# Kernel optimization log

Hardware: AMD Instinct MI355X
Metric: run time of the kernel (lower is better)

Reference implementation:

```python
import jax, jax.numpy as jnp
import numpy as np
import math

D_MODEL = 2048
NUM_HEADS = 32
NUM_KV_HEADS = 8
D_K = D_MODEL // NUM_HEADS  # 64
GROUPS = NUM_HEADS // NUM_KV_HEADS  # 4
WINDOW = 512
ROPE_BASE = 10000.0


def setup_inputs() -> dict:
    key = jax.random.key(0)
    ks = jax.random.split(key, 5)
    B, T = 2, 2048
    x = jax.random.normal(ks[0], (B, T, D_MODEL), dtype=jnp.float32)
    s = 0.02  # typical init scale to keep logits sane
    Wq = jax.random.normal(ks[1], (D_MODEL, D_MODEL), dtype=jnp.float32) * s
    Wk = jax.random.normal(ks[2], (NUM_KV_HEADS * D_K, D_MODEL), dtype=jnp.float32) * s
    Wv = jax.random.normal(ks[3], (NUM_KV_HEADS * D_K, D_MODEL), dtype=jnp.float32) * s
    Wo = jax.random.normal(ks[4], (D_MODEL, D_MODEL), dtype=jnp.float32) * s
    return {"x": x, "Wq": Wq, "Wk": Wk, "Wv": Wv, "Wo": Wo}


def _rotate_half(t):
    half = t.shape[-1] // 2
    return jnp.concatenate([-t[..., half:], t[..., :half]], axis=-1)


def _rope_cos_sin(T, dtype):
    inv_freq = 1.0 / (ROPE_BASE ** (jnp.arange(0, D_K, 2, dtype=jnp.float32) / D_K))
    pos = jnp.arange(T, dtype=jnp.float32)
    freqs = pos[:, None] * inv_freq[None, :]            # [T, D_K/2]
    emb = jnp.concatenate([freqs, freqs], axis=-1)       # [T, D_K]
    return jnp.cos(emb).astype(dtype)[None, None], jnp.sin(emb).astype(dtype)[None, None]


def reference(x, Wq, Wk, Wv, Wo):
    B, T, D = x.shape
    # Projections (nn.Linear: x @ W.T)
    Q = (x @ Wq.T).reshape(B, T, NUM_HEADS, D_K).transpose(0, 2, 1, 3)     # [B,H,T,dk]
    K = (x @ Wk.T).reshape(B, T, NUM_KV_HEADS, D_K).transpose(0, 2, 1, 3)  # [B,KV,T,dk]
    V = (x @ Wv.T).reshape(B, T, NUM_KV_HEADS, D_K).transpose(0, 2, 1, 3)
    # RoPE
    cos, sin = _rope_cos_sin(T, x.dtype)
    Q = Q * cos + _rotate_half(Q) * sin
    K = K * cos + _rotate_half(K) * sin
    # GQA: fold group dim into Q instead of repeat_interleave on K/V (same math)
    Qg = Q.reshape(B, NUM_KV_HEADS, GROUPS, T, D_K)
    scale = math.sqrt(D_K)
    scores = jnp.einsum('bhgqd,bhkd->bhgqk', Qg, K) / scale  # [B,KV,G,T,T]
    # sliding-window causal mask: valid iff 0 <= q_pos - k_pos < WINDOW
    pos = jnp.arange(T)
    dist = pos[:, None] - pos[None, :]
    win_mask = (dist < 0) | (dist >= WINDOW)
    scores = jnp.where(win_mask[None, None, None], -jnp.inf, scores)
    attn = jax.nn.softmax(scores, axis=-1)
    out = jnp.einsum('bhgqk,bhkd->bhgqd', attn, V)
    out = out.reshape(B, NUM_HEADS, T, D_K).transpose(0, 2, 1, 3).reshape(B, T, D)
    return out @ Wo.T
```

## Files before the change

kernel.cpp:

```cpp
#include <hip/hip_runtime.h>
#include <hip/hip_bf16.h>
#include <cstdint>
#include <cstddef>

typedef __attribute__((ext_vector_type(4))) float f32x4;
typedef __attribute__((ext_vector_type(8))) short bf16x8;
typedef __attribute__((ext_vector_type(4))) int i32x4;
typedef void __attribute__((address_space(1)))* as1_void_p;
typedef void __attribute__((address_space(3)))* as3_void_p;

#define T_SEQ 2048
#define D_MODEL 2048
#define NUM_HEADS 32
#define NUM_KV 8
#define GROUPS 4
#define DK 64
#define WINDOW 512
#define BATCH 2

#define NEG_BIG (-30000.0f)

__device__ __forceinline__ unsigned short f2b(float f) {
    unsigned int u = __builtin_bit_cast(unsigned int, f);
    u = (u + 0x7FFFu + ((u >> 16) & 1u)) >> 16;
    return (unsigned short)u;
}

__device__ __forceinline__ unsigned int cvtpk_bf16(float lo, float hi) {
    unsigned int r;
    asm("v_cvt_pk_bf16_f32 %0, %1, %2" : "=v"(r) : "v"(lo), "v"(hi));
    return r;
}

__device__ __forceinline__ void load_lds16(const void* g, void* l) {
    __builtin_amdgcn_global_load_lds((as1_void_p)(uintptr_t)g,
                                     (as3_void_p)(unsigned int)(uintptr_t)l,
                                     16, 0, 0);
}

#define CAST_N0 8388608
#define CAST_N1 12582912
#define CAST_N2 13631488
#define CAST_N3 14680064
#define CAST_N4 18874368
__global__ void cast_all_kernel(const float* __restrict__ x, const float* __restrict__ wq,
                                const float* __restrict__ wk, const float* __restrict__ wv,
                                const float* __restrict__ wo, unsigned short* __restrict__ dst) {
    int i = (blockIdx.x * blockDim.x + threadIdx.x) * 4;
    const int stride = gridDim.x * blockDim.x * 4;
    for (; i < CAST_N4; i += stride) {
        const float* src;
        int off;
        if (i < CAST_N0)      { src = x;  off = i; }
        else if (i < CAST_N1) { src = wq; off = i - CAST_N0; }
        else if (i < CAST_N2) { src = wk; off = i - CAST_N1; }
        else if (i < CAST_N3) { src = wv; off = i - CAST_N2; }
        else                  { src = wo; off = i - CAST_N3; }
        const float4 v = *(const float4*)(src + off);
        ushort4 o;
        o.x = f2b(v.x); o.y = f2b(v.y); o.z = f2b(v.z); o.w = f2b(v.w);
        *(ushort4*)(dst + i) = o;
    }
}

__global__ void rope_table_kernel(float* __restrict__ ct, float* __restrict__ st) {
    int i = blockIdx.x * blockDim.x + threadIdx.x;
    int t = i >> 5, j = i & 31;
    const float kln = 0.28782313662425556f;
    float inv = __expf(-(float)j * kln);
    if (j == 0) inv = 1.0f;
    float ang = (float)t * inv;
    float s, c;
    sincosf(ang, &s, &c);
    ct[i] = c; st[i] = s;
}

__global__ __launch_bounds__(512, 2) void gemm_qkv_rope(
    const unsigned short* __restrict__ A, const unsigned short* __restrict__ Bw,
    const float* __restrict__ ct, const float* __restrict__ st,
    unsigned short* __restrict__ Qb, unsigned short* __restrict__ Kb,
    unsigned short* __restrict__ Vt) {
    __shared__ __align__(16) unsigned short lds[65536];
    const int bid = blockIdx.x;
    const int xcd = bid & 7;
    const int l = bid >> 3;
    const int stl = l >> 2;
    const int w = l & 3;
    const int tile_m = xcd * 2 + (w >> 1);
    const int tile_n = stl * 2 + (w & 1);

    const int tid = threadIdx.x;
    const int lane = tid & 63;
    const int wid = tid >> 6;
    const int wr = wid >> 2, wc = wid & 3;
    const int lrow = lane & 15;
    const int g = lane >> 4;
    const int arow = tile_m * 256, brow = tile_n * 256;

    f32x4 acc[8][4] = {};

#define QSTAGE(SRC, ROWBASE, KCOL, USHOFF)                                     \
    { _Pragma("unroll") for (int u = 0; u < 2; ++u) {                          \
        const int gi = u * 512 + tid;                                          \
        const int row_ = gi >> 2, sl_ = gi & 3;                                \
        const int sc_ = (sl_ ^ ((row_ >> 1) & 3)) << 3;                        \
        load_lds16(SRC + (size_t)((ROWBASE) + row_) * 2048 + (KCOL) + sc_,     \
                   (char*)&lds[USHOFF] + gi * 16); } }

    QSTAGE(A, arow, 0,  0)     QSTAGE(Bw, brow, 0,  8192)
    QSTAGE(A, arow, 32, 16384) QSTAGE(Bw, brow, 32, 24576)
    QSTAGE(A, arow, 64, 32768) QSTAGE(Bw, brow, 64, 40960)
    asm volatile("s_waitcnt vmcnt(8)" ::: "memory");
    __builtin_amdgcn_sched_barrier(0);
    __builtin_amdgcn_s_barrier();

    for (int t = 0; t < 64; ++t) {
        const int cb = (t & 3) * 16384;
        const int sb = ((t + 3) & 3) * 16384;
        bf16x8 af[8], bfr[4];
#pragma unroll
        for (int m = 0; m < 8; ++m) {
            const int R = wr * 128 + m * 16 + lrow;
            af[m] = *(const bf16x8*)&lds[cb + R * 32 + ((g ^ ((R >> 1) & 3)) << 3)];
        }
#pragma unroll
        for (int n = 0; n < 4; ++n) {
            const int R = wc * 64 + n * 16 + lrow;
            bfr[n] = *(const bf16x8*)&lds[cb + 8192 + R * 32 + ((g ^ ((R >> 1) & 3)) << 3)];
        }
        if (t + 3 < 64) {
            QSTAGE(A, arow, (t + 3) * 32, sb)
            QSTAGE(Bw, brow, (t + 3) * 32, sb + 8192)
        }
        __builtin_amdgcn_s_setprio(1);
#pragma unroll
        for (int m = 0; m < 8; ++m)
#pragma unroll
            for (int n = 0; n < 4; ++n)
                acc[m][n] = __builtin_amdgcn_mfma_f32_16x16x32_bf16(af[m], bfr[n], acc[m][n], 0, 0, 0);
        __builtin_amdgcn_s_setprio(0);
        if (t < 61)      { asm volatile("s_waitcnt vmcnt(8)" ::: "memory"); }
        else if (t == 61){ asm volatile("s_waitcnt vmcnt(4)" ::: "memory"); }
        else             { asm volatile("s_waitcnt vmcnt(0)" ::: "memory"); }
        __builtin_amdgcn_sched_barrier(0);
        __builtin_amdgcn_s_barrier();
    }
#undef QSTAGE

    const int hcol = tile_n * 4 + wc;
#pragma unroll
    for (int m = 0; m < 8; ++m) {
        const int row0 = tile_m * 256 + wr * 128 + m * 16 + g * 4;
        const int bb = row0 >> 11;
        const int t0 = row0 & 2047;
        if (hcol < 40) {
            const bool isQ = (hcol < 32);
            const float sc = isQ ? 0.125f : 1.0f;
            unsigned short* base = isQ
                ? (Qb + ((size_t)(bb * NUM_HEADS + hcol) * T_SEQ) * 64)
                : (Kb + ((size_t)(bb * NUM_KV + (hcol - 32)) * T_SEQ) * 64);
#pragma unroll
            for (int r = 0; r < 4; ++r) {
                const int t = t0 + r;
                unsigned short* dst = base + (size_t)t * 64;
#pragma unroll
                for (int n = 0; n < 2; ++n) {
                    const int j = n * 16 + lrow;
                    const float c = ct[t * 32 + j], s = st[t * 32 + j];
                    const float v0 = acc[m][n][r], v1 = acc[m][n + 2][r];
                    dst[j]      = f2b((v0 * c - v1 * s) * sc);
                    dst[j + 32] = f2b((v1 * c + v0 * s) * sc);
                }
            }
        } else {
            const int vh = hcol - 40;
            const int chunk = t0 >> 5, tk = t0 & 31;
            unsigned short* cbase = Vt + ((size_t)(bb * NUM_KV + vh) * 64 + chunk) * 2048 + tk;
#pragma unroll
            for (int n = 0; n < 4; ++n) {
                const int d = n * 16 + lrow;
                unsigned int u0 = cvtpk_bf16(acc[m][n][0], acc[m][n][1]);
                unsigned int u1 = cvtpk_bf16(acc[m][n][2], acc[m][n][3]);
                uint2 val; val.x = u0; val.y = u1;
                *(uint2*)(cbase + d * 32) = val;
            }
        }
    }
}

__global__ __launch_bounds__(512, 2) void gemm_bf16_nt(
    const unsigned short* __restrict__ A, const unsigned short* __restrict__ B,
    float* __restrict__ C) {
    __shared__ __align__(16) unsigned short lds[49152];
    const int bid = blockIdx.x;
    const int xcd = bid & 7;
    const int l = bid >> 3;
    const int stl = l >> 4;
    const int w = l & 15;
    const int tmD = xcd * 4 + (w >> 2);
    const int tnD = stl * 4 + (w & 3);

    const int tid = threadIdx.x;
    const int lane = tid & 63;
    const int wid = tid >> 6;
    const int wr = wid >> 2, wc = wid & 3;
    const int lrow = lane & 15;
    const int g = lane >> 4;
    const int tile_m = tmD, tile_n = tnD;
    const int arow = tile_m * 128, brow = tile_n * 256;

    const int srow = tid >> 2, sslot = tid & 3;
    const int scol = (sslot ^ ((srow >> 1) & 3)) << 3;

    f32x4 acc[4][4] = {};

#define OSTAGE(BUF, KCOL)                                                      \
    {                                                                          \
        load_lds16(A + (size_t)(arow + srow) * 2048 + (KCOL) + scol,           \
                   (char*)&lds[(BUF) * 12288] + tid * 16);                     \
        _Pragma("unroll") for (int u = 0; u < 2; ++u) {                        \
            const int gi = u * 512 + tid;                                      \
            const int br_ = gi >> 2, bs_ = gi & 3;                             \
            const int bc_ = (bs_ ^ ((br_ >> 1) & 3)) << 3;                     \
            load_lds16(B + (size_t)(brow + br_) * 2048 + (KCOL) + bc_,         \
                       (char*)&lds[(BUF) * 12288 + 4096] + gi * 16);           \
        }                                                                      \
    }

    OSTAGE(0, 0) OSTAGE(1, 32) OSTAGE(2, 64)
    asm volatile("s_waitcnt vmcnt(6)" ::: "memory");
    __builtin_amdgcn_sched_barrier(0);
    __builtin_amdgcn_s_barrier();

    for (int t = 0; t < 64; ++t) {
        const int cb = (t & 3) * 12288;
        const int sb = (t + 3) & 3;
        bf16x8 af[4], bfr[4];
#pragma unroll
        for (int m = 0; m < 4; ++m) {
            const int R = wr * 64 + m * 16 + lrow;
            af[m] = *(const bf16x8*)&lds[cb + R * 32 + ((g ^ ((R >> 1) & 3)) << 3)];
        }
#pragma unroll
        for (int n = 0; n < 4; ++n) {
            const int R = wc * 64 + n * 16 + lrow;
            bfr[n] = *(const bf16x8*)&lds[cb + 4096 + R * 32 + ((g ^ ((R >> 1) & 3)) << 3)];
        }
        if (t + 3 < 64) OSTAGE(sb, (t + 3) * 32)
        __builtin_amdgcn_s_setprio(1);
#pragma unroll
        for (int m = 0; m < 4; ++m)
#pragma unroll
            for (int n = 0; n < 4; ++n)
                acc[m][n] = __builtin_amdgcn_mfma_f32_16x16x32_bf16(af[m], bfr[n], acc[m][n], 0, 0, 0);
        __builtin_amdgcn_s_setprio(0);
        if (t < 63) { asm volatile("s_waitcnt vmcnt(6)" ::: "memory"); }
        else        { asm volatile("s_waitcnt vmcnt(0)" ::: "memory"); }
        __builtin_amdgcn_sched_barrier(0);
        __builtin_amdgcn_s_barrier();
    }
#undef OSTAGE

#pragma unroll
    for (int m = 0; m < 4; ++m)
#pragma unroll
        for (int n = 0; n < 4; ++n) {
            const int col = tile_n * 256 + wc * 64 + n * 16 + lrow;
#pragma unroll
            for (int r = 0; r < 4; ++r) {
                const int row = tile_m * 128 + wr * 64 + m * 16 + g * 4 + r;
                C[(size_t)row * 2048 + col] = acc[m][n][r];
            }
        }
}

__global__ __launch_bounds__(512, 4) void attn_kernel(
    const unsigned short* __restrict__ Qb, const unsigned short* __restrict__ Kb,
    const unsigned short* __restrict__ Vt, unsigned short* __restrict__ Oout) {
    __shared__ __align__(16) unsigned short lds[16384];
    const int tid = threadIdx.x;
    const int lane = tid & 63;
    const int wv = tid >> 6;
    const int g4 = wv & 3;
    const int tile = wv >> 2;
    const int bid = blockIdx.x;
    const int kvh = bid & 7;
    const int b = (bid >> 3) & 1;
    const int band = 63 - (bid >> 4);
    const int q0A = band * 32;
    const int q0w = q0A + tile * 16;
    const int h = kvh * 4 + g4;

    const int lq = lane & 15;
    const int g = lane >> 4;
    const int kq8 = g * 8;
    const int q = q0w + lq;

    const unsigned short* Qrow = Qb + ((size_t)((b * NUM_HEADS + h) * T_SEQ) + q) * 64;
    const bf16x8 qf0 = *(const bf16x8*)(Qrow + kq8);
    const bf16x8 qf1 = *(const bf16x8*)(Qrow + 32 + kq8);

    f32x4 acc[4] = {};
    float lrun = 0.0f;

    int kc_lo = q0A - (WINDOW - 1);
    if (kc_lo < 0) kc_lo = 0;
    kc_lo &= ~31;
    const int N = ((q0A - kc_lo) >> 5) + 1;

    const unsigned short* Kg = Kb + (size_t)(b * NUM_KV + kvh) * T_SEQ * 64
                                  + (size_t)kc_lo * 64;
    const unsigned short* Vg = Vt + (size_t)(b * NUM_KV + kvh) * 64 * T_SEQ
                                  + (size_t)(kc_lo >> 5) * 2048;

    const int perm = (lq >> 2) * 8 + (lq & 3);
#define SWZK(r) (((r & 3) | ((r >> 3) << 2)) & 7)
    const int koff0 = perm * 64 + ((g ^ SWZK(perm)) << 3);
    const int koff1 = perm * 64 + (((4 + g) ^ SWZK(perm)) << 3);
    const int perm4 = perm + 4;
    const int koff2 = perm4 * 64 + ((g ^ SWZK(perm4)) << 3);
    const int koff3 = perm4 * 64 + (((4 + g) ^ SWZK(perm4)) << 3);
    int voff[4];
#pragma unroll
    for (int nd = 0; nd < 4; ++nd)
        voff[nd] = 2048 + (nd * 16 + lq) * 32 + ((g ^ ((lq >> 1) & 3)) << 3);

#define STAGE(T, BUF)                                                          \
    {                                                                          \
        if (tid < 256) {                                                       \
            const int row_ = tid >> 3, ps = tid & 7;                           \
            const int ls = ps ^ SWZK(row_);                                    \
            load_lds16(Kg + (size_t)(T) * 2048 + row_ * 64 + ls * 8,           \
                       (char*)lds + (BUF) * 8192 + tid * 16);                  \
        } else {                                                               \
            const int gi = tid - 256;                                          \
            const int row_ = gi >> 2, ps = gi & 3;                             \
            const int ls = ps ^ ((row_ >> 1) & 3);                             \
            load_lds16(Vg + (size_t)(T) * 2048 + row_ * 32 + ls * 8,           \
                       (char*)lds + (BUF) * 8192 + 4096 + gi * 16);            \
        }                                                                      \
    }

    STAGE(0, 0)
    if (N > 1) STAGE(1, 1)
    if (N > 2) STAGE(2, 2)
    if (N > 2)      { asm volatile("s_waitcnt vmcnt(2)" ::: "memory"); }
    else if (N > 1) { asm volatile("s_waitcnt vmcnt(1)" ::: "memory"); }
    else            { asm volatile("s_waitcnt vmcnt(0)" ::: "memory"); }
    __builtin_amdgcn_sched_barrier(0);
    __builtin_amdgcn_s_barrier();

    for (int t = 0; t < N; ++t) {
        const int kb = (t & 3) * 4096;
        bf16x8 kf[4], vf[4];
        kf[0] = *(const bf16x8*)&lds[kb + koff0];
        kf[1] = *(const bf16x8*)&lds[kb + koff1];
        kf[2] = *(const bf16x8*)&lds[kb + koff2];
        kf[3] = *(const bf16x8*)&lds[kb + koff3];
#pragma unroll
        for (int nd = 0; nd < 4; ++nd) vf[nd] = *(const bf16x8*)&lds[kb + voff[nd]];
        if (t + 3 < N) STAGE(t + 3, (t + 3) & 3)

        const int kc = kc_lo + t * 32;
        f32x4 st2[2] = {};
        st2[0] = __builtin_amdgcn_mfma_f32_16x16x32_bf16(kf[0], qf0, st2[0], 0, 0, 0);
        st2[0] = __builtin_amdgcn_mfma_f32_16x16x32_bf16(kf[1], qf1, st2[0], 0, 0, 0);
        st2[1] = __builtin_amdgcn_mfma_f32_16x16x32_bf16(kf[2], qf0, st2[1], 0, 0, 0);
        st2[1] = __builtin_amdgcn_mfma_f32_16x16x32_bf16(kf[3], qf1, st2[1], 0, 0, 0);

        float s8[8];
#pragma unroll
        for (int tt = 0; tt < 2; ++tt)
#pragma unroll
            for (int r = 0; r < 4; ++r) s8[tt * 4 + r] = st2[tt][r];

        if (kc < q0w - 496 || kc > q0w - 31) {
#pragma unroll
            for (int i = 0; i < 8; ++i) {
                const int key = kc + g * 8 + ((i >> 2) << 2) + (i & 3);
                const int dist = q - key;
                if (dist < 0 || dist >= WINDOW) s8[i] = NEG_BIG;
            }
        }

        float p8[8];
        float ps = 0.0f;
#pragma unroll
        for (int i = 0; i < 8; ++i) {
            p8[i] = __expf(s8[i]);
            ps += p8[i];
        }
        lrun += ps;

        i32x4 pwi;
        pwi[0] = (int)cvtpk_bf16(p8[0], p8[1]);
        pwi[1] = (int)cvtpk_bf16(p8[2], p8[3]);
        pwi[2] = (int)cvtpk_bf16(p8[4], p8[5]);
        pwi[3] = (int)cvtpk_bf16(p8[6], p8[7]);
        const bf16x8 pw = __builtin_bit_cast(bf16x8, pwi);

#pragma unroll
        for (int nd = 0; nd < 4; ++nd)
            acc[nd] = __builtin_amdgcn_mfma_f32_16x16x32_bf16(vf[nd], pw, acc[nd], 0, 0, 0);

        if (t + 1 < N) {
            if (t + 3 < N)      { asm volatile("s_waitcnt vmcnt(2)" ::: "memory"); }
            else if (t + 2 < N) { asm volatile("s_waitcnt vmcnt(1)" ::: "memory"); }
            else                { asm volatile("s_waitcnt vmcnt(0)" ::: "memory"); }
            __builtin_amdgcn_sched_barrier(0);
            __builtin_amdgcn_s_barrier();
        }
    }
#undef STAGE
#undef SWZK

    lrun += __shfl_xor(lrun, 16);
    lrun += __shfl_xor(lrun, 32);

    const float inv = 1.0f / lrun;
#pragma unroll
    for (int nd = 0; nd < 4; ++nd) {
        unsigned int u0 = cvtpk_bf16(acc[nd][0] * inv, acc[nd][1] * inv);
        unsigned int u1 = cvtpk_bf16(acc[nd][2] * inv, acc[nd][3] * inv);
        unsigned short* dst = Oout + ((size_t)(b * T_SEQ + q)) * D_MODEL + h * 64 + nd * 16 + g * 4;
        uint2 val; val.x = u0; val.y = u1;
        *(uint2*)dst = val;
    }
}

extern "C" void kernel_launch(void* const* d_in, const int* in_sizes, int n_in,
                              void* d_out, int out_size, void* d_ws, size_t ws_size,
                              hipStream_t stream) {
    const float* x = (const float*)d_in[0];
    const float* Wq = (const float*)d_in[1];
    const float* Wk = (const float*)d_in[2];
    const float* Wv = (const float*)d_in[3];
    const float* Wo = (const float*)d_in[4];
    float* out = (float*)d_out;

    char* ws = (char*)d_ws;
    size_t off = 0;
    auto alloc = [&](size_t bytes) -> char* {
        char* p = ws + off;
        off += (bytes + 255) & ~(size_t)255;
        return p;
    };
    unsigned short* xb   = (unsigned short*)alloc(8388608ull * 2);
    unsigned short* wcat = (unsigned short*)alloc(6291456ull * 2);
    unsigned short* wob  = (unsigned short*)alloc(4194304ull * 2);
    unsigned short* qb   = (unsigned short*)alloc(8388608ull * 2);
    unsigned short* kb   = (unsigned short*)alloc(2097152ull * 2);
    unsigned short* vt   = (unsigned short*)alloc(2097152ull * 2);
    unsigned short* attn = (unsigned short*)alloc(8388608ull * 2);
    float* ct            = (float*)alloc(65536ull * 4);
    float* st            = (float*)alloc(65536ull * 4);

    cast_all_kernel<<<2048, 256, 0, stream>>>(x, Wq, Wk, Wv, Wo, xb);
    rope_table_kernel<<<256, 256, 0, stream>>>(ct, st);

    gemm_qkv_rope<<<192, 512, 0, stream>>>(xb, wcat, ct, st, qb, kb, vt);

    attn_kernel<<<1024, 512, 0, stream>>>(qb, kb, vt, attn);

    gemm_bf16_nt<<<256, 512, 0, stream>>>(attn, wob, out);
}
```

Before: 148.3 us.

## Restructure QKV projection GEMM mainloop into 8-wave ping-pong with K=64 tiles

Replaces the 4-stage K=32 LDS ring in the QKV projection GEMM with a double-buffered K=64 scheme. Each buffer is split into 128-row halves that are refilled at a finer grain, interleaved with quarter-sized MFMA clusters and separated by barriers (a HipKittens-style 8-wave ping-pong). The LDS swizzle changes to an 8-slot XOR pattern for 64-wide rows. The goal is better overlap of global-to-LDS loads, LDS reads and MFMA, with fewer loop iterations. In exchange it adds many more s_barriers per iteration, and the prefetch depth drops from 3 stages to roughly one tile.

```diff
diff --git a/kernel.cpp b/kernel.cpp
--- a/kernel.cpp
+++ b/kernel.cpp
@@ -98,54 +98,115 @@
     const int arow = tile_m * 256, brow = tile_n * 256;
 
     f32x4 acc[8][4] = {};
-
-#define QSTAGE(SRC, ROWBASE, KCOL, USHOFF)                                     \
+    bf16x8 af0[8], af1[8], bf0[4], bf1[4];
+
+#define STAGEH(USHOFF, SRC, ROWBASE, KT)                                       \
     { _Pragma("unroll") for (int u = 0; u < 2; ++u) {                          \
         const int gi = u * 512 + tid;                                          \
-        const int row_ = gi >> 2, sl_ = gi & 3;                                \
-        const int sc_ = (sl_ ^ ((row_ >> 1) & 3)) << 3;                        \
-        load_lds16(SRC + (size_t)((ROWBASE) + row_) * 2048 + (KCOL) + sc_,     \
+        const int row_ = gi >> 3, sl_ = gi & 7;                                \
+        const int sc_ = (sl_ ^ (row_ & 7)) << 3;                               \
+        load_lds16(SRC + (size_t)((ROWBASE) + row_) * 2048 + (KT) * 64 + sc_,  \
                    (char*)&lds[USHOFF] + gi * 16); } }
 
-    QSTAGE(A, arow, 0,  0)     QSTAGE(Bw, brow, 0,  8192)
-    QSTAGE(A, arow, 32, 16384) QSTAGE(Bw, brow, 32, 24576)
-    QSTAGE(A, arow, 64, 32768) QSTAGE(Bw, brow, 64, 40960)
-    asm volatile("s_waitcnt vmcnt(8)" ::: "memory");
+#define RD_A(DST, BUF, KK)                                                     \
+    { _Pragma("unroll") for (int m = 0; m < 8; ++m) {                          \
+        const int R = m * 16 + lrow;                                           \
+        DST[m] = *(const bf16x8*)&lds[(BUF) + wr * 8192 + R * 64 +             \
+                                      ((((KK) * 4 + g) ^ (R & 7)) << 3)]; } }
+
+#define RD_B(BUF)                                                              \
+    { _Pragma("unroll") for (int n = 0; n < 4; ++n) {                          \
+        const int R = (wc & 1) * 64 + n * 16 + lrow;                           \
+        const int bb_ = (BUF) + 16384 + (wc >> 1) * 8192 + R * 64;             \
+        bf0[n] = *(const bf16x8*)&lds[bb_ + ((g ^ (R & 7)) << 3)];             \
+        bf1[n] = *(const bf16x8*)&lds[bb_ + (((4 + g) ^ (R & 7)) << 3)]; } }
+
+#define MM(AF, BF, NLO)                                                        \
+    { _Pragma("unroll") for (int m = 0; m < 8; ++m)                            \
+        _Pragma("unroll") for (int n = 0; n < 2; ++n)                          \
+            acc[m][(NLO) + n] = __builtin_amdgcn_mfma_f32_16x16x32_bf16(       \
+                AF[m], BF[(NLO) + n], acc[m][(NLO) + n], 0, 0, 0); }
+
+    STAGEH(0,     A,  arow,       0)
+    STAGEH(8192,  A,  arow + 128, 0)
+    STAGEH(16384, Bw, brow,       0)
+    STAGEH(24576, Bw, brow + 128, 0)
+    STAGEH(32768 + 16384, Bw, brow,       1)
+    STAGEH(32768 + 24576, Bw, brow + 128, 1)
+    STAGEH(32768 + 0,     A,  arow,       1)
+    asm volatile("s_waitcnt vmcnt(6)" ::: "memory");
     __builtin_amdgcn_sched_barrier(0);
     __builtin_amdgcn_s_barrier();
 
-    for (int t = 0; t < 64; ++t) {
-        const int cb = (t & 3) * 16384;
-        const int sb = ((t + 3) & 3) * 16384;
-        bf16x8 af[8], bfr[4];
-#pragma unroll
-        for (int m = 0; m < 8; ++m) {
-            const int R = wr * 128 + m * 16 + lrow;
-            af[m] = *(const bf16x8*)&lds[cb + R * 32 + ((g ^ ((R >> 1) & 3)) << 3)];
-        }
-#pragma unroll
-        for (int n = 0; n < 4; ++n) {
-            const int R = wc * 64 + n * 16 + lrow;
-            bfr[n] = *(const bf16x8*)&lds[cb + 8192 + R * 32 + ((g ^ ((R >> 1) & 3)) << 3)];
-        }
-        if (t + 3 < 64) {
-            QSTAGE(A, arow, (t + 3) * 32, sb)
-            QSTAGE(Bw, brow, (t + 3) * 32, sb + 8192)
-        }
-        __builtin_amdgcn_s_setprio(1);
-#pragma unroll
-        for (int m = 0; m < 8; ++m)
-#pragma unroll
-            for (int n = 0; n < 4; ++n)
-                acc[m][n] = __builtin_amdgcn_mfma_f32_16x16x32_bf16(af[m], bfr[n], acc[m][n], 0, 0, 0);
-        __builtin_amdgcn_s_setprio(0);
-        if (t < 61)      { asm volatile("s_waitcnt vmcnt(8)" ::: "memory"); }
-        else if (t == 61){ asm volatile("s_waitcnt vmcnt(4)" ::: "memory"); }
-        else             { asm volatile("s_waitcnt vmcnt(0)" ::: "memory"); }
+    for (int i = 0; i < 16; ++i) {
+        const int t0 = 2 * i;
+        const bool s02 = (t0 + 2 < 32);
+        const bool s13 = (t0 + 3 < 32);
+        RD_A(af0, 0, 0)
+        RD_B(0)
+        STAGEH(32768 + 8192, A, arow + 128, t0 + 1)
+        __builtin_amdgcn_s_barrier();
+        __builtin_amdgcn_s_setprio(1);
+        MM(af0, bf0, 0)
+        __builtin_amdgcn_s_setprio(0);
+        __builtin_amdgcn_s_barrier();
+        if (s02) STAGEH(16384, Bw, brow, t0 + 2)
+        __builtin_amdgcn_s_barrier();
+        __builtin_amdgcn_s_setprio(1);
+        MM(af0, bf0, 2)
+        __builtin_amdgcn_s_setprio(0);
+        __builtin_amdgcn_s_barrier();
+        RD_A(af1, 0, 1)
+        if (s02) STAGEH(24576, Bw, brow + 128, t0 + 2)
+        __builtin_amdgcn_s_barrier();
+        __builtin_amdgcn_s_setprio(1);
+        MM(af1, bf1, 0)
+        __builtin_amdgcn_s_setprio(0);
+        __builtin_amdgcn_s_barrier();
+        if (s02) STAGEH(0, A, arow, t0 + 2)
+        __builtin_amdgcn_s_barrier();
+        __builtin_amdgcn_s_setprio(1);
+        MM(af1, bf1, 2)
+        __builtin_amdgcn_s_setprio(0);
+        if (i < 15) { asm volatile("s_waitcnt vmcnt(6)" ::: "memory"); }
+        else        { asm volatile("s_waitcnt vmcnt(0)" ::: "memory"); }
         __builtin_amdgcn_sched_barrier(0);
         __builtin_amdgcn_s_barrier();
-    }
-#undef QSTAGE
+        RD_A(af0, 32768, 0)
+        RD_B(32768)
+        if (s02) STAGEH(8192, A, arow + 128, t0 + 2)
+        __builtin_amdgcn_s_barrier();
+        __builtin_amdgcn_s_setprio(1);
+        MM(af0, bf0, 0)
+        __builtin_amdgcn_s_setprio(0);
+        __builtin_amdgcn_s_barrier();
+        if (s13) STAGEH(32768 + 16384, Bw, brow, t0 + 3)
+        __builtin_amdgcn_s_barrier();
+        __builtin_amdgcn_s_setprio(1);
+        MM(af0, bf0, 2)
+        __builtin_amdgcn_s_setprio(0);
+        __builtin_amdgcn_s_barrier();
+        RD_A(af1, 32768, 1)
+        if (s13) STAGEH(32768 + 24576, Bw, brow + 128, t0 + 3)
+        __builtin_amdgcn_s_barrier();
+        __builtin_amdgcn_s_setprio(1);
+        MM(af1, bf1, 0)
+        __builtin_amdgcn_s_setprio(0);
+        __builtin_amdgcn_s_barrier();
+        if (s13) STAGEH(32768, A, arow, t0 + 3)
+        __builtin_amdgcn_s_barrier();
+        __builtin_amdgcn_s_setprio(1);
+        MM(af1, bf1, 2)
+        __builtin_amdgcn_s_setprio(0);
+        if (i < 15) { asm volatile("s_waitcnt vmcnt(6)" ::: "memory"); }
+        else        { asm volatile("s_waitcnt vmcnt(0)" ::: "memory"); }
+        __builtin_amdgcn_sched_barrier(0);
+        __builtin_amdgcn_s_barrier();
+    }
+#undef STAGEH
+#undef RD_A
+#undef RD_B
+#undef MM
 
     const int hcol = tile_n * 4 + wc;
 #pragma unroll
```

Result: no change. 149.7 us (+0.9%).
